# Kernel optimization log

Measured on AMD Instinct MI355X. Metric: run time of the kernel, lower is better.

The kernel has to match this reference:

```python
import jax, jax.numpy as jnp
import numpy as np

B, S, D, H = 4, 2048, 512, 8
HD = D // H  # head_dim = 64


def setup_inputs() -> dict:
    key = jax.random.key(0)
    ks = jax.random.split(key, 11)
    sc = 1.0 / np.sqrt(D)
    inp = {
        "query": jax.random.normal(ks[0], (B, S, D), jnp.float32),
        "key": jax.random.normal(ks[1], (B, S, D), jnp.float32),
        "value": jax.random.normal(ks[2], (B, S, D), jnp.float32),
        "Wq": jax.random.normal(ks[3], (D, D), jnp.float32) * sc,
        "bq": jax.random.normal(ks[4], (D,), jnp.float32) * sc,
        "Wk": jax.random.normal(ks[5], (D, D), jnp.float32) * sc,
        "bk": jax.random.normal(ks[6], (D,), jnp.float32) * sc,
        "Wv": jax.random.normal(ks[7], (D, D), jnp.float32) * sc,
        "bv": jax.random.normal(ks[8], (D,), jnp.float32) * sc,
        "Wo": jax.random.normal(ks[9], (D, D), jnp.float32) * sc,
        "bo": jax.random.normal(ks[10], (D,), jnp.float32) * sc,
    }
    return inp


def reference(query, key, value, Wq, bq, Wk, bk, Wv, bv, Wo, bo):
    batch = query.shape[0]
    # Linear projections (x @ W + b)
    q = query @ Wq + bq
    k = key @ Wk + bk
    v = value @ Wv + bv
    # NOTE: original uses .view(B*H, -1, head_dim) — a raw row-major reshape
    # (interleaves seq and head dims). Replicated exactly with jnp.reshape.
    q = q.reshape(batch * H, -1, HD)
    k = k.reshape(batch * H, -1, HD)
    v = v.reshape(batch * H, -1, HD)
    # scores: [B*H, L, L], fully materialized as in the original bmm path
    scores = jnp.einsum("bqd,bkd->bqk", q, k) / jnp.sqrt(jnp.float32(HD))
    probs = jax.nn.softmax(scores, axis=-1)  # dropout=0.0 -> identity
    out = jnp.einsum("bqk,bkd->bqd", probs, v)
    out = out.reshape(batch, -1, D)
    out = out @ Wo + bo
    return out, probs
```

## Files before the change

### kernel.cpp

```cpp
#include <hip/hip_runtime.h>


typedef __attribute__((ext_vector_type(4))) float fvec4;
typedef __attribute__((ext_vector_type(4))) float f32x4;
typedef __attribute__((ext_vector_type(8))) short bf16x8;
typedef __attribute__((ext_vector_type(4))) short bf16x4;

__device__ inline unsigned short f2bf_rne(float x) {
    unsigned u = __builtin_bit_cast(unsigned, x);
    unsigned r = (u + 0x7FFFu + ((u >> 16) & 1u)) >> 16;
    return (unsigned short)r;
}
__device__ inline float bf2f(unsigned short h) {
    unsigned u = ((unsigned)h) << 16;
    return __builtin_bit_cast(float, u);
}

__global__ __launch_bounds__(256) void split3(
    const float* __restrict__ X0, const float* __restrict__ X1, const float* __restrict__ X2,
    unsigned short* __restrict__ Hb, unsigned short* __restrict__ Lb)
{
    const float* X = blockIdx.z == 0 ? X0 : blockIdx.z == 1 ? X1 : X2;
    unsigned short* H = Hb + (long long)blockIdx.z * 4194304;
    unsigned short* L = Lb + (long long)blockIdx.z * 4194304;
    const long long i = (long long)(blockIdx.x * 256 + threadIdx.x) * 8;
    fvec4 a = *(const fvec4*)(X + i);
    fvec4 b = *(const fvec4*)(X + i + 4);
    bf16x8 h, l;
#pragma unroll
    for (int j = 0; j < 4; j++) {
        unsigned short hh = f2bf_rne(a[j]);
        h[j] = (short)hh; l[j] = (short)f2bf_rne(a[j] - bf2f(hh));
        hh = f2bf_rne(b[j]);
        h[4 + j] = (short)hh; l[4 + j] = (short)f2bf_rne(b[j] - bf2f(hh));
    }
    *(bf16x8*)(H + i) = h;
    *(bf16x8*)(L + i) = l;
}

__global__ __launch_bounds__(256) void wtrans_split(
    const float* __restrict__ W0, const float* __restrict__ W1,
    const float* __restrict__ W2, const float* __restrict__ W3,
    unsigned short* __restrict__ TH, unsigned short* __restrict__ TL)
{
    const float* W = blockIdx.z == 0 ? W0 : blockIdx.z == 1 ? W1 : blockIdx.z == 2 ? W2 : W3;
    unsigned short* th = TH + (long long)blockIdx.z * 262144;
    unsigned short* tl = TL + (long long)blockIdx.z * 262144;
    __shared__ float t[32][33];
    const int x = threadIdx.x, y = threadIdx.y;
    const int n0 = blockIdx.x * 32, k0 = blockIdx.y * 32;
#pragma unroll
    for (int j = 0; j < 4; j++) t[y + 8 * j][x] = W[(long long)(k0 + y + 8 * j) * 512 + n0 + x];
    __syncthreads();
#pragma unroll
    for (int j = 0; j < 4; j++) {
        float v = t[x][y + 8 * j];
        unsigned short h = f2bf_rne(v);
        th[(long long)(n0 + y + 8 * j) * 512 + k0 + x] = h;
        tl[(long long)(n0 + y + 8 * j) * 512 + k0 + x] = f2bf_rne(v - bf2f(h));
    }
}

template <bool SPLIT_OUT>
__global__ __launch_bounds__(256) void gemm_bs(
    const unsigned short* __restrict__ AH, const unsigned short* __restrict__ AL, long long sAz,
    const unsigned short* __restrict__ BH, const unsigned short* __restrict__ BL, long long sBz,
    const float* __restrict__ b0, const float* __restrict__ b1, const float* __restrict__ b2,
    unsigned short* __restrict__ OH, unsigned short* __restrict__ OL,
    float* __restrict__ OF, long long sOz)
{
    __shared__ __align__(16) unsigned short Ah[64][40];
    __shared__ __align__(16) unsigned short Al[64][40];
    __shared__ __align__(16) unsigned short Bh[64][40];
    __shared__ __align__(16) unsigned short Bl[64][40];

    const int tid = threadIdx.x, lane = tid & 63, wv = tid >> 6;
    const int z = blockIdx.z;
    AH += z * sAz; AL += z * sAz; BH += z * sBz; BL += z * sBz;
    const float* bias = z == 0 ? b0 : z == 1 ? b1 : b2;
    const int row0 = blockIdx.x * 64, col0 = blockIdx.y * 64;

    f32x4 acc[4];
#pragma unroll
    for (int i = 0; i < 4; i++)
#pragma unroll
        for (int r = 0; r < 4; r++) acc[i][r] = 0.f;

    const int lr = tid >> 2;
    const int lc = (tid & 3) * 8;
    const int ar = (wv << 4) + (lane & 15);
    const int kk = (lane >> 4) << 3;

    bf16x8 ra_h, ra_l, rb_h, rb_l;
    auto ldregs = [&](int k0) {
        ra_h = *(const bf16x8*)(AH + (long long)(row0 + lr) * 512 + k0 + lc);
        ra_l = *(const bf16x8*)(AL + (long long)(row0 + lr) * 512 + k0 + lc);
        rb_h = *(const bf16x8*)(BH + (long long)(col0 + lr) * 512 + k0 + lc);
        rb_l = *(const bf16x8*)(BL + (long long)(col0 + lr) * 512 + k0 + lc);
    };

    ldregs(0);
    for (int t = 0; t < 16; t++) {
        __syncthreads();
        *(bf16x8*)&Ah[lr][lc] = ra_h;
        *(bf16x8*)&Al[lr][lc] = ra_l;
        *(bf16x8*)&Bh[lr][lc] = rb_h;
        *(bf16x8*)&Bl[lr][lc] = rb_l;
        if (t < 15) ldregs((t + 1) * 32);
        __syncthreads();

        bf16x8 aH = *(const bf16x8*)&Ah[ar][kk];
        bf16x8 aL = *(const bf16x8*)&Al[ar][kk];
#pragma unroll
        for (int cb = 0; cb < 4; cb++) {
            const int br = (cb << 4) + (lane & 15);
            bf16x8 bH = *(const bf16x8*)&Bh[br][kk];
            bf16x8 bL = *(const bf16x8*)&Bl[br][kk];
            acc[cb] = __builtin_amdgcn_mfma_f32_16x16x32_bf16(aH, bH, acc[cb], 0, 0, 0);
            acc[cb] = __builtin_amdgcn_mfma_f32_16x16x32_bf16(aH, bL, acc[cb], 0, 0, 0);
            acc[cb] = __builtin_amdgcn_mfma_f32_16x16x32_bf16(aL, bH, acc[cb], 0, 0, 0);
        }
    }

#pragma unroll
    for (int cb = 0; cb < 4; cb++) {
#pragma unroll
        for (int r = 0; r < 4; r++) {
            const long long row = row0 + (wv << 4) + ((lane >> 4) << 2) + r;
            const int col = col0 + (cb << 4) + (lane & 15);
            float val = acc[cb][r] + bias[col];
            if constexpr (SPLIT_OUT) {
                unsigned short h = f2bf_rne(val);
                (OH + z * sOz)[row * 512 + col] = h;
                if (z != 2)
                    (OL + z * sOz)[row * 512 + col] = f2bf_rne(val - bf2f(h));
            } else {
                (OF + z * sOz)[row * 512 + col] = val;
            }
        }
    }
}

__global__ __launch_bounds__(256) void vtrans2(
    const unsigned short* __restrict__ vh, unsigned short* __restrict__ vt)
{
    __shared__ __align__(16) unsigned short t[64][80];
    const int tid = threadIdx.x;
    const int c = blockIdx.y;
    const int l0 = blockIdx.x * 64;
    const long long cb = (long long)c * 131072;
    const int rrow = tid >> 3, ccol = (tid & 7) * 8;
#pragma unroll
    for (int rr = 0; rr < 2; rr++)
        *(bf16x8*)&t[rrow + rr * 32][ccol] =
            *(const bf16x8*)(vh + cb + (long long)(l0 + rrow + rr * 32) * 64 + ccol);
    __syncthreads();
#pragma unroll
    for (int rr = 0; rr < 2; rr++) {
        const int hd = rrow + rr * 32;
        bf16x8 o;
#pragma unroll
        for (int q2 = 0; q2 < 8; q2++) o[q2] = (short)t[ccol + q2][hd];
        *(bf16x8*)(vt + cb + (long long)hd * 2048 + l0 + ccol) = o;
    }
}

__global__ __launch_bounds__(256) void fused_attn(
    const unsigned short* __restrict__ qh, const unsigned short* __restrict__ ql,
    const unsigned short* __restrict__ kh, const unsigned short* __restrict__ kl,
    const unsigned short* __restrict__ vt,
    float* __restrict__ probs,
    unsigned short* __restrict__ aoh, unsigned short* __restrict__ aol)
{
    __shared__ __align__(16) unsigned short skh[64][80];
    __shared__ __align__(16) unsigned short skl[64][80];
    __shared__ __align__(16) unsigned short svt[64][80];
    __shared__ __align__(16) unsigned short sP[4][16][68];

    const int tid = threadIdx.x, lane = tid & 63, wv = tid >> 6;

    const int orig = blockIdx.y * 32 + blockIdx.x;
    const int myid = (orig & 7) * 128 + (orig >> 3);
    const int c    = myid >> 5;
    const int row0 = (myid & 31) * 64;
    const long long cbase = (long long)c * 131072;

    const int l15 = lane & 15, g = lane >> 4, kk = g * 8;
    const int srow = tid >> 3;
    const int scol = (tid & 7) * 8;
    const int p_r0 = g * 4;

    const int arow = row0 + wv * 16 + l15;
    bf16x8 aH[2], aL[2];
    {
        const unsigned short* qp  = qh + cbase + (long long)arow * 64;
        const unsigned short* qlp = ql + cbase + (long long)arow * 64;
        aH[0] = *(const bf16x8*)(qp + kk);   aH[1] = *(const bf16x8*)(qp + 32 + kk);
        aL[0] = *(const bf16x8*)(qlp + kk);  aL[1] = *(const bf16x8*)(qlp + 32 + kk);
    }

    bf16x8 rkh[2], rkl[2], rvt[2];
    auto ld1 = [&](int j) {
        const long long ktb = cbase + (long long)j * 4096;
        const long long vtb = cbase + j * 64;
#pragma unroll
        for (int rr = 0; rr < 2; rr++) {
            const int r2 = srow + rr * 32;
            rkh[rr] = *(const bf16x8*)(kh + ktb + (long long)r2 * 64 + scol);
            rkl[rr] = *(const bf16x8*)(kl + ktb + (long long)r2 * 64 + scol);
            rvt[rr] = *(const bf16x8*)(vt + vtb + (long long)r2 * 2048 + scol);
        }
    };
    auto st1 = [&]() {
#pragma unroll
        for (int rr = 0; rr < 2; rr++) {
            const int r2 = srow + rr * 32;
            *(bf16x8*)&skh[r2][scol] = rkh[rr];
            *(bf16x8*)&skl[r2][scol] = rkl[rr];
            *(bf16x8*)&svt[r2][scol] = rvt[rr];
        }
    };
    auto ld2 = [&](int j) {
        const long long ktb = cbase + (long long)j * 4096;
#pragma unroll
        for (int rr = 0; rr < 2; rr++) {
            const int r2 = srow + rr * 32;
            rkh[rr] = *(const bf16x8*)(kh + ktb + (long long)r2 * 64 + scol);
            rkl[rr] = *(const bf16x8*)(kl + ktb + (long long)r2 * 64 + scol);
        }
    };
    auto st2 = [&]() {
#pragma unroll
        for (int rr = 0; rr < 2; rr++) {
            const int r2 = srow + rr * 32;
            *(bf16x8*)&skh[r2][scol] = rkh[rr];
            *(bf16x8*)&skl[r2][scol] = rkl[rr];
        }
    };

    f32x4 acc_o[4];
#pragma unroll
    for (int i = 0; i < 4; i++)
#pragma unroll
        for (int r = 0; r < 4; r++) acc_o[i][r] = 0.f;
    float rsum[4] = {0.f, 0.f, 0.f, 0.f};

    ld1(0);
    for (int j = 0; j < 32; j++) {
        __syncthreads();
        st1();
        if (j < 31) ld1(j + 1);
        __syncthreads();

        f32x4 s[4];
#pragma unroll
        for (int cb = 0; cb < 4; cb++)
#pragma unroll
            for (int r = 0; r < 4; r++) s[cb][r] = 0.f;
#pragma unroll
        for (int ks = 0; ks < 2; ks++) {
#pragma unroll
            for (int cb = 0; cb < 4; cb++) {
                const int col = cb * 16 + l15;
                bf16x8 bH = *(const bf16x8*)&skh[col][ks * 32 + kk];
                bf16x8 bL = *(const bf16x8*)&skl[col][ks * 32 + kk];
                s[cb] = __builtin_amdgcn_mfma_f32_16x16x32_bf16(aH[ks], bH, s[cb], 0, 0, 0);
                s[cb] = __builtin_amdgcn_mfma_f32_16x16x32_bf16(aH[ks], bL, s[cb], 0, 0, 0);
                s[cb] = __builtin_amdgcn_mfma_f32_16x16x32_bf16(aL[ks], bH, s[cb], 0, 0, 0);
            }
        }
#pragma unroll
        for (int cb = 0; cb < 4; cb++) {
#pragma unroll
            for (int r = 0; r < 4; r++) {
                float p = __expf(s[cb][r] * 0.125f);
                rsum[r] += p;
                sP[wv][p_r0 + r][cb * 16 + l15] = f2bf_rne(p);
            }
        }
#pragma unroll
        for (int ks = 0; ks < 2; ks++) {
            bf16x4 p0 = *(const bf16x4*)&sP[wv][l15][ks * 32 + kk];
            bf16x4 p1 = *(const bf16x4*)&sP[wv][l15][ks * 32 + kk + 4];
            bf16x8 pa;
#pragma unroll
            for (int q2 = 0; q2 < 4; q2++) { pa[q2] = p0[q2]; pa[4 + q2] = p1[q2]; }
#pragma unroll
            for (int co = 0; co < 4; co++) {
                bf16x8 bV = *(const bf16x8*)&svt[co * 16 + l15][ks * 32 + kk];
                acc_o[co] = __builtin_amdgcn_mfma_f32_16x16x32_bf16(pa, bV, acc_o[co], 0, 0, 0);
            }
        }
    }

#pragma unroll
    for (int r = 0; r < 4; r++) {
        float s = rsum[r];
        s += __shfl_xor(s, 1, 64);
        s += __shfl_xor(s, 2, 64);
        s += __shfl_xor(s, 4, 64);
        s += __shfl_xor(s, 8, 64);
        rsum[r] = 1.f / s;
    }

#pragma unroll
    for (int co = 0; co < 4; co++) {
#pragma unroll
        for (int r = 0; r < 4; r++) {
            const long long oi = cbase + (long long)(row0 + wv * 16 + p_r0 + r) * 64 + co * 16 + l15;
            float o = acc_o[co][r] * rsum[r];
            unsigned short h = f2bf_rne(o);
            aoh[oi] = h;
            aol[oi] = f2bf_rne(o - bf2f(h));
        }
    }

    ld2(0);
    for (int j = 0; j < 32; j++) {
        __syncthreads();
        st2();
        if (j < 31) ld2(j + 1);
        __syncthreads();

        f32x4 s[4];
#pragma unroll
        for (int cb = 0; cb < 4; cb++)
#pragma unroll
            for (int r = 0; r < 4; r++) s[cb][r] = 0.f;
#pragma unroll
        for (int ks = 0; ks < 2; ks++) {
#pragma unroll
            for (int cb = 0; cb < 4; cb++) {
                const int col = cb * 16 + l15;
                bf16x8 bH = *(const bf16x8*)&skh[col][ks * 32 + kk];
                bf16x8 bL = *(const bf16x8*)&skl[col][ks * 32 + kk];
                s[cb] = __builtin_amdgcn_mfma_f32_16x16x32_bf16(aH[ks], bH, s[cb], 0, 0, 0);
                s[cb] = __builtin_amdgcn_mfma_f32_16x16x32_bf16(aH[ks], bL, s[cb], 0, 0, 0);
                s[cb] = __builtin_amdgcn_mfma_f32_16x16x32_bf16(aL[ks], bH, s[cb], 0, 0, 0);
            }
        }
        float* pb = probs + (long long)c * 4194304 +
                    (long long)(row0 + wv * 16 + p_r0) * 2048 + j * 64;
#pragma unroll
        for (int cb = 0; cb < 4; cb++) {
#pragma unroll
            for (int r = 0; r < 4; r++) {
                pb[(long long)r * 2048 + cb * 16 + l15] = __expf(s[cb][r] * 0.125f) * rsum[r];
            }
        }
    }
}

extern "C" void kernel_launch(void* const* d_in, const int* in_sizes, int n_in,
                              void* d_out, int out_size, void* d_ws, size_t ws_size,
                              hipStream_t stream)
{
    const float* query = (const float*)d_in[0];
    const float* key_  = (const float*)d_in[1];
    const float* value = (const float*)d_in[2];
    const float* Wq = (const float*)d_in[3];
    const float* bq = (const float*)d_in[4];
    const float* Wk = (const float*)d_in[5];
    const float* bk = (const float*)d_in[6];
    const float* Wv = (const float*)d_in[7];
    const float* bv = (const float*)d_in[8];
    const float* Wo = (const float*)d_in[9];
    const float* bo = (const float*)d_in[10];

    float* out   = (float*)d_out;
    float* probs = out + 4194304LL;

    unsigned short* XH = (unsigned short*)probs;
    unsigned short* XL = XH + 3 * 4194304LL;

    const long long MiB = 1LL << 20;
    char* w = (char*)d_ws;
    unsigned short* QKVH = (unsigned short*)(w + 0 * MiB);
    unsigned short* QKVL = (unsigned short*)(w + 24 * MiB);
    unsigned short* WTH  = (unsigned short*)(w + 40 * MiB);
    unsigned short* WTL  = (unsigned short*)(w + 42 * MiB);
    unsigned short* VT   = (unsigned short*)(w + 44 * MiB);
    unsigned short* AOH  = (unsigned short*)(w + 52 * MiB);
    unsigned short* AOL  = (unsigned short*)(w + 60 * MiB);

    split3<<<dim3(2048, 1, 3), 256, 0, stream>>>(query, key_, value, XH, XL);
    wtrans_split<<<dim3(16, 16, 4), dim3(32, 8, 1), 0, stream>>>(Wq, Wk, Wv, Wo, WTH, WTL);

    gemm_bs<true><<<dim3(128, 8, 3), 256, 0, stream>>>(
        XH, XL, 4194304, WTH, WTL, 262144, bq, bk, bv,
        QKVH, QKVL, nullptr, 4194304);

    vtrans2<<<dim3(32, 32, 1), 256, 0, stream>>>(QKVH + 2 * 4194304LL, VT);

    fused_attn<<<dim3(32, 32, 1), 256, 0, stream>>>(
        QKVH, QKVL, QKVH + 4194304LL, QKVL + 4194304LL, VT, probs, AOH, AOL);

    gemm_bs<false><<<dim3(128, 8, 1), 256, 0, stream>>>(
        AOH, AOL, 0, WTH + 3 * 262144LL, WTL + 3 * 262144LL, 0, bo, bo, bo,
        nullptr, nullptr, out, 0);
}
```

Before: 313.2 us.

## Rewrite split-bf16 GEMM with 128x128 tiles, direct global-to-LDS loads, double buffering

The projection GEMMs move from 64x64 to 128x128 output tiles, with each wave computing a 64x64 sub-tile of 4x4 MFMA blocks to raise operand reuse. Tiles are staged with global_load_lds straight into double-buffered, XOR-swizzled LDS, so the register round trip goes away and the next K-slice loads while the current one computes. In exchange there are fewer blocks (768 for QKV, 256 for the output projection), more accumulator registers per thread, and more LDS per block, which can lower occupancy.

After: 297.9 us. 4.9% less time.

```diff
diff --git a/kernel.cpp b/kernel.cpp
--- a/kernel.cpp
+++ b/kernel.cpp
@@ -6,6 +6,13 @@
 typedef __attribute__((ext_vector_type(8))) short bf16x8;
 typedef __attribute__((ext_vector_type(4))) short bf16x4;
 
+typedef const __attribute__((address_space(1))) unsigned int* gas_t;
+typedef __attribute__((address_space(3))) unsigned int* las_t;
+
+__device__ inline void gl_lds16(const void* g, void* l) {
+    __builtin_amdgcn_global_load_lds((gas_t)g, (las_t)l, 16, 0, 0);
+}
+
 __device__ inline unsigned short f2bf_rne(float x) {
     unsigned u = __builtin_bit_cast(unsigned, x);
     unsigned r = (u + 0x7FFFu + ((u >> 16) & 1u)) >> 16;
@@ -15,6 +22,8 @@
     unsigned u = ((unsigned)h) << 16;
     return __builtin_bit_cast(float, u);
 }
+
+__device__ inline int fo4(int row, int ch) { return row * 32 + ((ch ^ ((row >> 1) & 3)) * 8); }
 
 __global__ __launch_bounds__(256) void split3(
     const float* __restrict__ X0, const float* __restrict__ X1, const float* __restrict__ X2,
@@ -62,80 +71,96 @@
 }
 
 template <bool SPLIT_OUT>
-__global__ __launch_bounds__(256) void gemm_bs(
+__global__ __launch_bounds__(256) void gemm_split(
     const unsigned short* __restrict__ AH, const unsigned short* __restrict__ AL, long long sAz,
     const unsigned short* __restrict__ BH, const unsigned short* __restrict__ BL, long long sBz,
     const float* __restrict__ b0, const float* __restrict__ b1, const float* __restrict__ b2,
     unsigned short* __restrict__ OH, unsigned short* __restrict__ OL,
     float* __restrict__ OF, long long sOz)
 {
-    __shared__ __align__(16) unsigned short Ah[64][40];
-    __shared__ __align__(16) unsigned short Al[64][40];
-    __shared__ __align__(16) unsigned short Bh[64][40];
-    __shared__ __align__(16) unsigned short Bl[64][40];
+    __shared__ __align__(16) unsigned short sAh[2][4096];
+    __shared__ __align__(16) unsigned short sAl[2][4096];
+    __shared__ __align__(16) unsigned short sBh[2][4096];
+    __shared__ __align__(16) unsigned short sBl[2][4096];
 
     const int tid = threadIdx.x, lane = tid & 63, wv = tid >> 6;
     const int z = blockIdx.z;
     AH += z * sAz; AL += z * sAz; BH += z * sBz; BL += z * sBz;
     const float* bias = z == 0 ? b0 : z == 1 ? b1 : b2;
-    const int row0 = blockIdx.x * 64, col0 = blockIdx.y * 64;
-
-    f32x4 acc[4];
-#pragma unroll
-    for (int i = 0; i < 4; i++)
-#pragma unroll
-        for (int r = 0; r < 4; r++) acc[i][r] = 0.f;
-
-    const int lr = tid >> 2;
-    const int lc = (tid & 3) * 8;
-    const int ar = (wv << 4) + (lane & 15);
-    const int kk = (lane >> 4) << 3;
-
-    bf16x8 ra_h, ra_l, rb_h, rb_l;
-    auto ldregs = [&](int k0) {
-        ra_h = *(const bf16x8*)(AH + (long long)(row0 + lr) * 512 + k0 + lc);
-        ra_l = *(const bf16x8*)(AL + (long long)(row0 + lr) * 512 + k0 + lc);
-        rb_h = *(const bf16x8*)(BH + (long long)(col0 + lr) * 512 + k0 + lc);
-        rb_l = *(const bf16x8*)(BL + (long long)(col0 + lr) * 512 + k0 + lc);
+    const int row0 = blockIdx.x * 128, col0 = blockIdx.y * 128;
+    const int wr = wv >> 1, wc = wv & 1;
+    const int l15 = lane & 15, g = lane >> 4;
+
+    const unsigned short* src = wv == 0 ? AH + (long long)row0 * 512
+                              : wv == 1 ? AL + (long long)row0 * 512
+                              : wv == 2 ? BH + (long long)col0 * 512
+                              :           BL + (long long)col0 * 512;
+    unsigned short* dst = wv == 0 ? &sAh[0][0] : wv == 1 ? &sAl[0][0]
+                        : wv == 2 ? &sBh[0][0] : &sBl[0][0];
+    const int srow = lane >> 2;
+    const int csrc = (lane & 3) ^ ((lane >> 3) & 3);
+
+    f32x4 acc[4][4];
+#pragma unroll
+    for (int a = 0; a < 4; a++)
+#pragma unroll
+        for (int b = 0; b < 4; b++)
+#pragma unroll
+            for (int r = 0; r < 4; r++) acc[a][b][r] = 0.f;
+
+    auto stage = [&](int buf, int k0) {
+#pragma unroll
+        for (int i = 0; i < 8; i++) {
+            gl_lds16(src + (long long)(i * 16 + srow) * 512 + k0 + csrc * 8,
+                     dst + buf * 4096 + i * 512);
+        }
     };
 
-    ldregs(0);
+    stage(0, 0);
+    __syncthreads();
+    int cur = 0;
     for (int t = 0; t < 16; t++) {
+        if (t < 15) stage(cur ^ 1, (t + 1) * 32);
+        bf16x8 aHf[4], aLf[4];
+#pragma unroll
+        for (int rb = 0; rb < 4; rb++) {
+            const int r = wr * 64 + rb * 16 + l15;
+            aHf[rb] = *(const bf16x8*)&sAh[cur][fo4(r, g)];
+            aLf[rb] = *(const bf16x8*)&sAl[cur][fo4(r, g)];
+        }
+#pragma unroll
+        for (int cb = 0; cb < 4; cb++) {
+            const int rB = wc * 64 + cb * 16 + l15;
+            bf16x8 bH = *(const bf16x8*)&sBh[cur][fo4(rB, g)];
+            bf16x8 bL = *(const bf16x8*)&sBl[cur][fo4(rB, g)];
+#pragma unroll
+            for (int rb = 0; rb < 4; rb++) {
+                acc[rb][cb] = __builtin_amdgcn_mfma_f32_16x16x32_bf16(aHf[rb], bH, acc[rb][cb], 0, 0, 0);
+                acc[rb][cb] = __builtin_amdgcn_mfma_f32_16x16x32_bf16(aHf[rb], bL, acc[rb][cb], 0, 0, 0);
+                acc[rb][cb] = __builtin_amdgcn_mfma_f32_16x16x32_bf16(aLf[rb], bH, acc[rb][cb], 0, 0, 0);
+            }
+        }
         __syncthreads();
-        *(bf16x8*)&Ah[lr][lc] = ra_h;
-        *(bf16x8*)&Al[lr][lc] = ra_l;
-        *(bf16x8*)&Bh[lr][lc] = rb_h;
-        *(bf16x8*)&Bl[lr][lc] = rb_l;
-        if (t < 15) ldregs((t + 1) * 32);
-        __syncthreads();
-
-        bf16x8 aH = *(const bf16x8*)&Ah[ar][kk];
-        bf16x8 aL = *(const bf16x8*)&Al[ar][kk];
+        cur ^= 1;
+    }
+
+#pragma unroll
+    for (int rb = 0; rb < 4; rb++) {
 #pragma unroll
         for (int cb = 0; cb < 4; cb++) {
-            const int br = (cb << 4) + (lane & 15);
-            bf16x8 bH = *(const bf16x8*)&Bh[br][kk];
-            bf16x8 bL = *(const bf16x8*)&Bl[br][kk];
-            acc[cb] = __builtin_amdgcn_mfma_f32_16x16x32_bf16(aH, bH, acc[cb], 0, 0, 0);
-            acc[cb] = __builtin_amdgcn_mfma_f32_16x16x32_bf16(aH, bL, acc[cb], 0, 0, 0);
-            acc[cb] = __builtin_amdgcn_mfma_f32_16x16x32_bf16(aL, bH, acc[cb], 0, 0, 0);
-        }
-    }
-
-#pragma unroll
-    for (int cb = 0; cb < 4; cb++) {
-#pragma unroll
-        for (int r = 0; r < 4; r++) {
-            const long long row = row0 + (wv << 4) + ((lane >> 4) << 2) + r;
-            const int col = col0 + (cb << 4) + (lane & 15);
-            float val = acc[cb][r] + bias[col];
-            if constexpr (SPLIT_OUT) {
-                unsigned short h = f2bf_rne(val);
-                (OH + z * sOz)[row * 512 + col] = h;
-                if (z != 2)
-                    (OL + z * sOz)[row * 512 + col] = f2bf_rne(val - bf2f(h));
-            } else {
-                (OF + z * sOz)[row * 512 + col] = val;
+            const int col = col0 + wc * 64 + cb * 16 + l15;
+#pragma unroll
+            for (int rr = 0; rr < 4; rr++) {
+                const long long row = row0 + wr * 64 + rb * 16 + g * 4 + rr;
+                float val = acc[rb][cb][rr] + bias[col];
+                if constexpr (SPLIT_OUT) {
+                    unsigned short h = f2bf_rne(val);
+                    (OH + z * sOz)[row * 512 + col] = h;
+                    if (z != 2)
+                        (OL + z * sOz)[row * 512 + col] = f2bf_rne(val - bf2f(h));
+                } else {
+                    (OF + z * sOz)[row * 512 + col] = val;
+                }
             }
         }
     }
@@ -386,7 +411,7 @@
     split3<<<dim3(2048, 1, 3), 256, 0, stream>>>(query, key_, value, XH, XL);
     wtrans_split<<<dim3(16, 16, 4), dim3(32, 8, 1), 0, stream>>>(Wq, Wk, Wv, Wo, WTH, WTL);
 
-    gemm_bs<true><<<dim3(128, 8, 3), 256, 0, stream>>>(
+    gemm_split<true><<<dim3(64, 4, 3), 256, 0, stream>>>(
         XH, XL, 4194304, WTH, WTL, 262144, bq, bk, bv,
         QKVH, QKVL, nullptr, 4194304);
 
@@ -395,7 +420,7 @@
     fused_attn<<<dim3(32, 32, 1), 256, 0, stream>>>(
         QKVH, QKVL, QKVH + 4194304LL, QKVL + 4194304LL, VT, probs, AOH, AOL);
 
-    gemm_bs<false><<<dim3(128, 8, 1), 256, 0, stream>>>(
+    gemm_split<false><<<dim3(64, 4, 1), 256, 0, stream>>>(
         AOH, AOL, 0, WTH + 3 * 262144LL, WTL + 3 * 262144LL, 0, bo, bo, bo,
         nullptr, nullptr, out, 0);
 }
```
